# Kernel tuning notes

Measured on AMD Instinct MI355X. Metric: run time of the kernel, lower is better.

Reference implementation:

```python
import jax, jax.numpy as jnp
import numpy as np

DIM = 2048
HEAD = 256
SEQ = 4096

def setup_inputs() -> dict:
    key = jax.random.key(0)
    ks = jax.random.split(key, 7)
    s = 1.0 / np.sqrt(DIM)
    return {
        "marketStateBatch": jax.random.normal(ks[0], (SEQ, DIM), dtype=jnp.float32),
        "Wq": jax.random.uniform(ks[1], (HEAD, DIM), jnp.float32, -s, s),
        "bq": jax.random.uniform(ks[2], (HEAD,), jnp.float32, -s, s),
        "Wk": jax.random.uniform(ks[3], (HEAD, DIM), jnp.float32, -s, s),
        "bk": jax.random.uniform(ks[4], (HEAD,), jnp.float32, -s, s),
        "Wv": jax.random.uniform(ks[5], (HEAD, DIM), jnp.float32, -s, s),
        "bv": jax.random.uniform(ks[6], (HEAD,), jnp.float32, -s, s),
    }

def reference(marketStateBatch, Wq, bq, Wk, bk, Wv, bv):
    x = marketStateBatch  # [S, D]
    q = x @ Wq.T + bq     # [S, H]
    k = x @ Wk.T + bk     # [S, H]
    v = x @ Wv.T + bv     # [S, H]
    # NOTE: original scales by sqrt(dimensionSize), the INPUT dim, not head dim.
    scores = (q @ k.T) * (1.0 / np.sqrt(DIM))  # [S, S]
    S = x.shape[0]
    causal = jnp.tril(jnp.ones((S, S), dtype=bool))
    scores = jnp.where(causal, scores, -jnp.inf)
    attn = jax.nn.softmax(scores, axis=-1)
    # torch.nan_to_num(attn, 0.0): rows are never all -inf here (diag kept),
    # but replicate the op faithfully.
    attn = jnp.nan_to_num(attn, nan=0.0)
    return attn @ v  # [S, H]
```

## Files before the change

kernel.cpp:

```cpp
#include <hip/hip_runtime.h>
#include <stdint.h>

#define SEQ 4096
#define DIMK 2048
#define HD 256

typedef __attribute__((ext_vector_type(8))) short bf16x8;
typedef __attribute__((ext_vector_type(4))) short u16x4;
typedef __attribute__((ext_vector_type(4))) float f32x4;
typedef __attribute__((ext_vector_type(16))) float f32x16;
typedef unsigned short u16;
typedef unsigned int u32;

#define BAR() asm volatile("s_barrier" ::: "memory")
#define VMCNT(n) asm volatile("s_waitcnt vmcnt(" #n ")" ::: "memory")

__device__ __forceinline__ u16 f2bf(float f) {
    u32 u = __float_as_uint(f);
    u += 0x7FFFu + ((u >> 16) & 1u);
    return (u16)(u >> 16);
}

__device__ __forceinline__ float bf2f(u16 h) {
    u32 u = ((u32)h) << 16;
    return __uint_as_float(u);
}

__device__ __forceinline__ bf16x8 pack8(f32x4 a0, f32x4 a1) {
    bf16x8 v8;
    v8[0]=(short)f2bf(a0[0]); v8[1]=(short)f2bf(a0[1]);
    v8[2]=(short)f2bf(a0[2]); v8[3]=(short)f2bf(a0[3]);
    v8[4]=(short)f2bf(a1[0]); v8[5]=(short)f2bf(a1[1]);
    v8[6]=(short)f2bf(a1[2]); v8[7]=(short)f2bf(a1[3]);
    return v8;
}

__device__ __forceinline__ void gl16(const void* g, void* l) {
    __builtin_amdgcn_global_load_lds(
        (const __attribute__((address_space(1))) void*)g,
        (__attribute__((address_space(3))) void*)l, 16, 0, 0);
}

__device__ __forceinline__ u32 cvtpk(float lo, float hi) {
    u32 d;
    asm("v_cvt_pk_bf16_f32 %0, %1, %2" : "=v"(d) : "v"(lo), "v"(hi));
    return d;
}

__device__ __forceinline__ void plswap(u32& x, u32& y) {
#if __has_builtin(__builtin_amdgcn_permlane32_swap)
    typedef int i32x2 __attribute__((ext_vector_type(2)));
    i32x2 r = __builtin_amdgcn_permlane32_swap((int)x, (int)y, false, false);
    x = (u32)r[0]; y = (u32)r[1];
#else
    asm("v_permlane32_swap_b32 %0, %1" : "+v"(x), "+v"(y));
#endif
}

__global__ __launch_bounds__(256) void cvt_all2(
    const float* __restrict__ x, const float* __restrict__ Wq,
    const float* __restrict__ Wk, const float* __restrict__ Wv,
    u16* __restrict__ xb_sw, u16* __restrict__ wb_sw)
{
    const int y = blockIdx.y;
    int i = blockIdx.x * 256 + threadIdx.x;
    int stride = gridDim.x * 256;
    if (y == 0) {
        for (; i < SEQ*DIMK/8; i += stride) {
            int row = i >> 8, c8 = i & 255;
            f32x4 a0 = *(const f32x4*)(x + (size_t)row*DIMK + c8*8);
            f32x4 a1 = *(const f32x4*)(x + (size_t)row*DIMK + c8*8 + 4);
            int mt = row >> 6, rl = row & 63, kt = c8 >> 3, sl = c8 & 7;
            size_t dst = ((size_t)(mt*32 + kt))*4096 + rl*64 + ((sl ^ (rl&7))*8);
            *(bf16x8*)(xb_sw + dst) = pack8(a0, a1);
        }
    } else {
        const float* W = (y==1) ? Wq : (y==2) ? Wk : Wv;
        for (; i < HD*DIMK/8; i += stride) {
            int row = i >> 8, c8 = i & 255;
            f32x4 a0 = *(const f32x4*)(W + (size_t)row*DIMK + c8*8);
            f32x4 a1 = *(const f32x4*)(W + (size_t)row*DIMK + c8*8 + 4);
            int gr = (y-1)*256 + row;
            int nt = gr >> 7, rl = gr & 127, kt = c8 >> 3, sl = c8 & 7;
            size_t dst = ((size_t)(nt*32 + kt))*8192 + rl*64 + ((sl ^ (rl&7))*8);
            *(bf16x8*)(wb_sw + dst) = pack8(a0, a1);
        }
    }
}

__global__ __launch_bounds__(256, 2) void qkv_gemm2b(
    const u16* __restrict__ xb_sw, const u16* __restrict__ wb_sw,
    const float* __restrict__ bq, const float* __restrict__ bk,
    const float* __restrict__ bv,
    u16* __restrict__ qb, u16* __restrict__ kb_t, u16* __restrict__ vt_t)
{
    __shared__ char T[3][24576];

    const int tid = threadIdx.x;
    const int lane = tid & 63;
    const int w = tid >> 6;
    const int r = lane & 15, g = lane >> 4;
    const int wr = w >> 1, wc = w & 1;
    const int mt = blockIdx.x;
    const int y  = blockIdx.y;
    const int z  = y >> 1;
    const float* bias = (z==0) ? bq : (z==1) ? bk : bv;

    const u16* abase = xb_sw + (size_t)mt*32*4096;
    const u16* bbase = wb_sw + (size_t)y*32*8192;

    f32x4 zero = {0.f,0.f,0.f,0.f};
    f32x4 acc[2][4];
    #pragma unroll
    for (int m = 0; m < 2; ++m)
        #pragma unroll
        for (int n = 0; n < 4; ++n) acc[m][n] = zero;

    auto stage = [&](int b, int kt) {
        const u16* ag = abase + (size_t)kt*4096 + w*1024 + lane*8;
        const u16* bg = bbase + (size_t)kt*8192 + w*2048 + lane*8;
        char* al = T[b] + w*2048;
        char* bl = T[b] + 8192 + w*4096;
        gl16(ag,        al);
        gl16(ag + 512,  al + 1024);
        gl16(bg,        bl);
        gl16(bg + 512,  bl + 1024);
        gl16(bg + 1024, bl + 2048);
        gl16(bg + 1536, bl + 3072);
    };

    stage(0, 0);
    stage(1, 1);

    for (int kt = 0; kt < 32; ++kt) {
        if (kt < 31) { VMCNT(6); } else { VMCNT(0); }
        BAR();
        if (kt + 2 < 32) stage((kt + 2) % 3, kt + 2);
        const char* A = T[kt % 3];
        const char* B = T[kt % 3] + 8192;
        __builtin_amdgcn_s_setprio(1);
        #pragma unroll
        for (int kc = 0; kc < 2; ++kc) {
            bf16x8 af[2], bfr[4];
            #pragma unroll
            for (int m = 0; m < 2; ++m) {
                int arow = wr*32 + m*16 + r;
                af[m] = *(const bf16x8*)(A + arow*128 + (((kc*4+g) ^ (arow&7)) << 4));
            }
            #pragma unroll
            for (int n = 0; n < 4; ++n) {
                int brow = wc*64 + n*16 + r;
                bfr[n] = *(const bf16x8*)(B + brow*128 + (((kc*4+g) ^ (brow&7)) << 4));
            }
            #pragma unroll
            for (int m = 0; m < 2; ++m)
                #pragma unroll
                for (int n = 0; n < 4; ++n)
                    acc[m][n] = __builtin_amdgcn_mfma_f32_16x16x32_bf16(
                        af[m], bfr[n], acc[m][n], 0, 0, 0);
        }
        __builtin_amdgcn_s_setprio(0);
    }

    const int m0 = mt*64, n0 = y*128;
    const float qs = 0.03187936f;
    if (z == 0) {
        #pragma unroll
        for (int n = 0; n < 4; ++n) {
            int hc = (n0 + wc*64 + n*16 + r) & 255;
            float bcol = bias[hc];
            #pragma unroll
            for (int m = 0; m < 2; ++m) {
                int row0 = m0 + wr*32 + m*16 + g*4;
                #pragma unroll
                for (int j = 0; j < 4; ++j)
                    qb[(size_t)(row0+j)*HD + hc] = f2bf((acc[m][n][j] + bcol) * qs);
            }
        }
    } else if (z == 1) {
        #pragma unroll
        for (int n = 0; n < 4; ++n) {
            int hc = (n0 + wc*64 + n*16 + r) & 255;
            float bcol = bias[hc];
            #pragma unroll
            for (int m = 0; m < 2; ++m) {
                int row0 = m0 + wr*32 + m*16 + g*4;
                #pragma unroll
                for (int j = 0; j < 4; ++j) {
                    int rowj = row0 + j;
                    int t = rowj >> 5, rl = rowj & 31;
                    kb_t[(size_t)t*8192 + rl*256 + (((hc>>3) ^ (rl&7))*8) + (hc&7)]
                        = f2bf(acc[m][n][j] + bcol);
                }
            }
        }
    } else {
        #pragma unroll
        for (int n = 0; n < 4; ++n) {
            int hc = (n0 + wc*64 + n*16 + r) & 255;
            float bcol = bias[hc];
            #pragma unroll
            for (int m = 0; m < 2; ++m) {
                int kv0 = m0 + wr*32 + m*16 + g*4;
                int t = kv0 >> 5, kl = kv0 & 31;
                u16x4 pk;
                #pragma unroll
                for (int j = 0; j < 4; ++j) pk[j] = (short)f2bf(acc[m][n][j] + bcol);
                *(u16x4*)(vt_t + (size_t)t*8192 + hc*32 +
                          (((kl>>3) ^ (hc&3) ^ ((hc>>2)&3))*8) + (kl&7)) = pk;
            }
        }
    }
}

__global__ __launch_bounds__(256, 2) void attn_part10(
    const u16* __restrict__ qb, const u16* __restrict__ kb_t,
    const u16* __restrict__ vt_t,
    u16* __restrict__ po, float* __restrict__ pm, float* __restrict__ pl,
    int C)
{
    __shared__ char Kb[2][16384];
    __shared__ char Vb[2][16384];

    const int pid = blockIdx.x;
    int Q = 0, a0 = 0;
    for (int k = 0; k < 32; ++k) {
        int nsk = (4*k + 4 + C - 1) / C;
        if (pid < a0 + nsk) { Q = k; break; }
        a0 += nsk;
    }
    const int s  = pid - a0;
    const int nt = 4*Q + 4;
    const int t0 = s*C;
    const int t1 = min(t0 + C, nt);

    const int tid = threadIdx.x;
    const int L = tid & 63;
    const int w = tid >> 6;
    const int l31 = L & 31;
    const int h   = L >> 5;
    const int qg  = Q*128 + w*32 + l31;
    const int vsw = (l31 & 3) ^ ((l31 >> 2) & 3);
    const int kx  = l31 & 7;

    auto stageK = [&](int t, int b) {
        const u16* kg = kb_t + (size_t)t*8192 + w*2048 + L*8;
        char* kl = Kb[b] + w*4096;
        #pragma unroll
        for (int i = 0; i < 4; ++i) gl16(kg + i*512, kl + i*1024);
    };
    auto stageV = [&](int t, int b) {
        const u16* vg = vt_t + (size_t)t*8192 + w*2048 + L*8;
        char* vl = Vb[b] + w*4096;
        #pragma unroll
        for (int i = 0; i < 4; ++i) gl16(vg + i*512, vl + i*1024);
    };

    stageK(t0, t0 & 1);
    stageK(min(t0 + 1, t1 - 1), (t0 + 1) & 1);
    stageV(t0, t0 & 1);

    bf16x8 qf[16];
    {
        const u16* qp = qb + (size_t)qg*HD + h*8;
        #pragma unroll
        for (int c = 0; c < 16; ++c) qf[c] = *(const bf16x8*)(qp + c*16);
    }

    f32x16 o[8];
    #pragma unroll
    for (int ht = 0; ht < 8; ++ht)
        #pragma unroll
        for (int e = 0; e < 16; ++e) o[ht][e] = 0.f;
    float lsum = 0.f;
    bf16x8 pp0, pp1;

    auto finish_tile = [&](f32x16& sv, int t) {
        if (t*32 + 31 > Q*128 + w*32) {
            #pragma unroll
            for (int e = 0; e < 16; ++e) {
                int kvr = (e & 3) + 8*(e >> 2) + 4*h;
                if (t*32 + kvr > qg) sv[e] = -__builtin_inff();
            }
        }
        #pragma unroll
        for (int e = 0; e < 16; ++e) sv[e] = exp2f(sv[e]);
        float r0 = ((sv[0]+sv[1])+(sv[2]+sv[3])) + ((sv[4]+sv[5])+(sv[6]+sv[7]));
        float r1 = ((sv[8]+sv[9])+(sv[10]+sv[11])) + ((sv[12]+sv[13])+(sv[14]+sv[15]));
        lsum += r0 + r1;
        {
            union { u32 wd[4]; bf16x8 v8; } up;
            u32 A = cvtpk(sv[0],  sv[1]),  B = cvtpk(sv[2],  sv[3]);
            u32 Cc= cvtpk(sv[4],  sv[5]),  D = cvtpk(sv[6],  sv[7]);
            plswap(A, Cc); plswap(B, D);
            up.wd[0]=A; up.wd[1]=B; up.wd[2]=Cc; up.wd[3]=D;
            pp0 = up.v8;
        }
        {
            union { u32 wd[4]; bf16x8 v8; } up;
            u32 A1 = cvtpk(sv[8],  sv[9]),  B1 = cvtpk(sv[10], sv[11]);
            u32 C1 = cvtpk(sv[12], sv[13]), D1 = cvtpk(sv[14], sv[15]);
            plswap(A1, C1); plswap(B1, D1);
            up.wd[0]=A1; up.wd[1]=B1; up.wd[2]=C1; up.wd[3]=D1;
            pp1 = up.v8;
        }
    };

    {
        VMCNT(8);
        BAR();
        const char* K = Kb[t0 & 1];
        #define LDK(c) (*(const bf16x8*)(K + l31*512 + (((2*(c) + h) ^ kx) << 4)))
        f32x16 sv;
        #pragma unroll
        for (int e = 0; e < 16; ++e) sv[e] = 0.f;
        __builtin_amdgcn_s_setprio(1);
        {
            bf16x8 kk0 = LDK(0), kk1 = LDK(1);
            #pragma unroll
            for (int c = 0; c < 16; ++c) {
                bf16x8 kc = (c & 1) ? kk1 : kk0;
                sv = __builtin_amdgcn_mfma_f32_32x32x16_bf16(kc, qf[c], sv, 0, 0, 0);
                if (c + 2 < 16) { if (c & 1) kk1 = LDK(c + 2); else kk0 = LDK(c + 2); }
            }
        }
        #undef LDK
        __builtin_amdgcn_s_setprio(0);
        finish_tile(sv, t0);
        BAR();
        stageK(min(t0 + 2, t1 - 1), t0 & 1);
        stageV(min(t0 + 1, t1 - 1), (t0 + 1) & 1);
    }

    for (int t = t0 + 1; t < t1; ++t) {
        VMCNT(8);
        BAR();
        const char* K  = Kb[t & 1];
        const char* Vp = Vb[(t - 1) & 1];

        #define LDK(c) (*(const bf16x8*)(K + l31*512 + (((2*(c) + h) ^ kx) << 4)))
        f32x16 sv;
        #pragma unroll
        for (int e = 0; e < 16; ++e) sv[e] = 0.f;
        __builtin_amdgcn_s_setprio(1);
        {
            bf16x8 kk0 = LDK(0), kk1 = LDK(1);
            #pragma unroll
            for (int c = 0; c < 16; ++c) {
                bf16x8 kc = (c & 1) ? kk1 : kk0;
                sv = __builtin_amdgcn_mfma_f32_32x32x16_bf16(kc, qf[c], sv, 0, 0, 0);
                if (c + 2 < 16) { if (c & 1) kk1 = LDK(c + 2); else kk0 = LDK(c + 2); }
                {
                    const int ht = c & 7;
                    const int sl = ((c < 8) ? h : (2 + h)) ^ vsw;
                    bf16x8 vf = *(const bf16x8*)(Vp + (ht*32 + l31)*64 + (sl << 4));
                    o[ht] = __builtin_amdgcn_mfma_f32_32x32x16_bf16(
                        vf, (c < 8) ? pp0 : pp1, o[ht], 0, 0, 0);
                }
            }
        }
        #undef LDK
        __builtin_amdgcn_s_setprio(0);

        finish_tile(sv, t);

        BAR();
        stageK(min(t + 2, t1 - 1), t & 1);
        stageV(min(t + 1, t1 - 1), (t + 1) & 1);
    }

    VMCNT(0);
    BAR();
    {
        const char* Vp = Vb[(t1 - 1) & 1];
        __builtin_amdgcn_s_setprio(1);
        #pragma unroll
        for (int ht = 0; ht < 8; ++ht) {
            bf16x8 vf0 = *(const bf16x8*)(Vp + (ht*32 + l31)*64 + (((h)     ^ vsw) << 4));
            bf16x8 vf1 = *(const bf16x8*)(Vp + (ht*32 + l31)*64 + (((2 + h) ^ vsw) << 4));
            o[ht] = __builtin_amdgcn_mfma_f32_32x32x16_bf16(vf0, pp0, o[ht], 0, 0, 0);
            o[ht] = __builtin_amdgcn_mfma_f32_32x32x16_bf16(vf1, pp1, o[ht], 0, 0, 0);
        }
        __builtin_amdgcn_s_setprio(0);
    }

    float lrun = lsum + __shfl_xor(lsum, 32);
    if (h == 0) {
        pm[(size_t)pid*128 + w*32 + l31] = 0.f;
        pl[(size_t)pid*128 + w*32 + l31] = lrun;
    }
    u16* op = po + ((size_t)pid*128 + w*32 + l31) * 256;
    #pragma unroll
    for (int ht = 0; ht < 8; ++ht)
        #pragma unroll
        for (int j = 0; j < 8; ++j) {
            u32 pk = (u32)f2bf(o[ht][2*j]) | ((u32)f2bf(o[ht][2*j+1]) << 16);
            int hdb = ht*32 + (j & 1)*2 + (j >> 1)*8 + 4*h;
            *(u32*)(op + hdb) = pk;
        }
}

__global__ __launch_bounds__(256) void attn_combine5(
    const u16* __restrict__ po, const float* __restrict__ pm,
    const float* __restrict__ pl, float* __restrict__ out, int C)
{
    const int tid = threadIdx.x;
    const int row = blockIdx.x * 16 + (tid >> 4);
    const int cg  = tid & 15;
    const int Q   = row >> 7, rr = row & 127;
    const int nt  = 4*Q + 4;
    const int ns  = (nt + C - 1) / C;
    int pid0 = 0;
    for (int k = 0; k < Q; ++k) pid0 += (4*k + 4 + C - 1) / C;

    float M = -1e30f;
    for (int s = 0; s < ns; ++s)
        M = fmaxf(M, pm[(size_t)(pid0+s)*128 + rr]);

    float lt = 0.f;
    f32x4 acc[4];
    f32x4 zero = {0.f,0.f,0.f,0.f};
    #pragma unroll
    for (int v = 0; v < 4; ++v) acc[v] = zero;

    for (int s = 0; s < ns; ++s) {
        float ms  = pm[(size_t)(pid0+s)*128 + rr];
        float wgt = exp2f(ms - M);
        lt += wgt * pl[(size_t)(pid0+s)*128 + rr];
        const u16* p = po + ((size_t)(pid0+s)*128 + rr)*256 + cg*16;
        #pragma unroll
        for (int v = 0; v < 4; ++v) {
            u16x4 pv = *(const u16x4*)(p + v*4);
            #pragma unroll
            for (int e = 0; e < 4; ++e)
                acc[v][e] += wgt * bf2f((u16)pv[e]);
        }
    }
    float inv = 1.f / lt;
    f32x4* op = (f32x4*)(out + (size_t)row*256 + cg*16);
    #pragma unroll
    for (int v = 0; v < 4; ++v) op[v] = acc[v] * inv;
}

extern "C" void kernel_launch(void* const* d_in, const int* in_sizes, int n_in,
                              void* d_out, int out_size, void* d_ws, size_t ws_size,
                              hipStream_t stream) {
    const float* x  = (const float*)d_in[0];
    const float* Wq = (const float*)d_in[1];
    const float* bq = (const float*)d_in[2];
    const float* Wk = (const float*)d_in[3];
    const float* bk = (const float*)d_in[4];
    const float* Wv = (const float*)d_in[5];
    const float* bv = (const float*)d_in[6];
    float* out = (float*)d_out;

    const size_t xb_bytes  = (size_t)SEQ * DIMK * 2;
    const size_t wb_bytes  = (size_t)768 * DIMK * 2;
    const size_t qkv_bytes = (size_t)SEQ * HD * 2;
    const size_t base = xb_bytes + wb_bytes + 3*qkv_bytes;

    int C = 64;
    size_t npid = 0;
    const int cand[4] = {5, 8, 16, 64};
    for (int ci = 0; ci < 4; ++ci) {
        int c = cand[ci];
        size_t np = 0;
        for (int k = 0; k < 32; ++k) np += (size_t)(4*k + 4 + c - 1) / c;
        size_t need = base + np * ((size_t)128*256*2 + 2*128*4);
        if (need <= ws_size) { C = c; npid = np; break; }
        if (ci == 3) { C = c; npid = np; }
    }

    char* p = (char*)d_ws;
    u16* xb_sw = (u16*)p; p += xb_bytes;
    u16* wb_sw = (u16*)p; p += wb_bytes;
    u16* qbuf  = (u16*)p; p += qkv_bytes;
    u16* kb_t  = (u16*)p; p += qkv_bytes;
    u16* vt_t  = (u16*)p; p += qkv_bytes;
    u16* po    = (u16*)p; p += npid * 128 * 256 * 2;
    float* pm  = (float*)p; p += npid * 128 * 4;
    float* pl  = (float*)p; p += npid * 128 * 4;

    cvt_all2<<<dim3(512, 4), 256, 0, stream>>>(x, Wq, Wk, Wv, xb_sw, wb_sw);

    qkv_gemm2b<<<dim3(SEQ/64, 6), 256, 0, stream>>>(
        xb_sw, wb_sw, bq, bk, bv, qbuf, kb_t, vt_t);

    attn_part10<<<(int)npid, 256, 0, stream>>>(
        qbuf, kb_t, vt_t, po, pm, pl, C);

    attn_combine5<<<SEQ/16, 256, 0, stream>>>(po, pm, pl, out, C);
}
```

Measured before the change: 75.94 us.

## Replace split-KV partial writes and combine with float atomics into transposed accumulator

Each split-KV partition now atomically adds its unnormalized output and row sum straight into a transposed fp32 accumulator, instead of writing bf16 partials plus max and sum for a separate combine pass. A zeroing kernel and a small normalize/transpose kernel replace the combine kernel, and C is fixed to 5. The aim is to cut partial-buffer traffic and the combine work. The cost is many float atomics per element plus an extra zeroing launch. The atomics also make the result order-nondeterministic, though that is safe here only because the fixed max of zero makes the partials directly summable.

Result: slower. 119.5 us (+57.3%).

```diff
diff --git a/kernel.cpp b/kernel.cpp
--- a/kernel.cpp
+++ b/kernel.cpp
@@ -19,11 +19,6 @@
     u32 u = __float_as_uint(f);
     u += 0x7FFFu + ((u >> 16) & 1u);
     return (u16)(u >> 16);
-}
-
-__device__ __forceinline__ float bf2f(u16 h) {
-    u32 u = ((u32)h) << 16;
-    return __uint_as_float(u);
 }
 
 __device__ __forceinline__ bf16x8 pack8(f32x4 a0, f32x4 a1) {
@@ -55,6 +50,22 @@
 #else
     asm("v_permlane32_swap_b32 %0, %1" : "+v"(x), "+v"(y));
 #endif
+}
+
+__device__ __forceinline__ void atomadd(float* p, float v) {
+    unsafeAtomicAdd(p, v);
+}
+
+__global__ __launch_bounds__(256) void zero_buf(float* __restrict__ ot,
+                                                float* __restrict__ pl)
+{
+    const int n4 = (HD*SEQ)/4;
+    f32x4 z = {0.f,0.f,0.f,0.f};
+    int i = blockIdx.x * 256 + threadIdx.x;
+    int stride = gridDim.x * 256;
+    for (; i < n4; i += stride) *(f32x4*)(ot + (size_t)i*4) = z;
+    for (i = blockIdx.x * 256 + threadIdx.x; i < SEQ/4; i += stride)
+        *(f32x4*)(pl + (size_t)i*4) = z;
 }
 
 __global__ __launch_bounds__(256) void cvt_all2(
@@ -213,10 +224,10 @@
     }
 }
 
-__global__ __launch_bounds__(256, 2) void attn_part10(
+__global__ __launch_bounds__(256, 2) void attn_part12(
     const u16* __restrict__ qb, const u16* __restrict__ kb_t,
     const u16* __restrict__ vt_t,
-    u16* __restrict__ po, float* __restrict__ pm, float* __restrict__ pl,
+    float* __restrict__ ot, float* __restrict__ pl,
     int C)
 {
     __shared__ char Kb[2][16384];
@@ -384,62 +395,47 @@
         __builtin_amdgcn_s_setprio(0);
     }
 
-    float lrun = lsum + __shfl_xor(lsum, 32);
-    if (h == 0) {
-        pm[(size_t)pid*128 + w*32 + l31] = 0.f;
-        pl[(size_t)pid*128 + w*32 + l31] = lrun;
-    }
-    u16* op = po + ((size_t)pid*128 + w*32 + l31) * 256;
+    atomadd(&pl[qg], lsum);
     #pragma unroll
     for (int ht = 0; ht < 8; ++ht)
         #pragma unroll
-        for (int j = 0; j < 8; ++j) {
-            u32 pk = (u32)f2bf(o[ht][2*j]) | ((u32)f2bf(o[ht][2*j+1]) << 16);
-            int hdb = ht*32 + (j & 1)*2 + (j >> 1)*8 + 4*h;
-            *(u32*)(op + hdb) = pk;
-        }
-}
-
-__global__ __launch_bounds__(256) void attn_combine5(
-    const u16* __restrict__ po, const float* __restrict__ pm,
-    const float* __restrict__ pl, float* __restrict__ out, int C)
+        for (int e = 0; e < 16; ++e) {
+            int hd = ht*32 + (e & 3) + 8*(e >> 2) + 4*h;
+            atomadd(ot + (size_t)hd*SEQ + qg, o[ht][e]);
+        }
+}
+
+__global__ __launch_bounds__(256) void attn_norm(
+    const float* __restrict__ ot, const float* __restrict__ pl,
+    float* __restrict__ out)
 {
-    const int tid = threadIdx.x;
-    const int row = blockIdx.x * 16 + (tid >> 4);
-    const int cg  = tid & 15;
-    const int Q   = row >> 7, rr = row & 127;
-    const int nt  = 4*Q + 4;
-    const int ns  = (nt + C - 1) / C;
-    int pid0 = 0;
-    for (int k = 0; k < Q; ++k) pid0 += (4*k + 4 + C - 1) / C;
-
-    float M = -1e30f;
-    for (int s = 0; s < ns; ++s)
-        M = fmaxf(M, pm[(size_t)(pid0+s)*128 + rr]);
-
-    float lt = 0.f;
-    f32x4 acc[4];
-    f32x4 zero = {0.f,0.f,0.f,0.f};
+    __shared__ float tr[64][257];
+    const int tid  = threadIdx.x;
+    const int row0 = blockIdx.x * 64;
+    const int rl = tid & 63;
+    const int hq = tid >> 6;
+
+    #pragma unroll 4
+    for (int h2 = 0; h2 < 64; ++h2) {
+        int hd = hq*64 + h2;
+        tr[rl][hd] = ot[(size_t)hd*SEQ + row0 + rl];
+    }
+    __syncthreads();
+
+    const int orow = tid >> 2;
+    const int c0   = (tid & 3) * 64;
+    float inv = 1.f / pl[row0 + orow];
+    float* op = out + (size_t)(row0 + orow)*HD + c0;
     #pragma unroll
-    for (int v = 0; v < 4; ++v) acc[v] = zero;
-
-    for (int s = 0; s < ns; ++s) {
-        float ms  = pm[(size_t)(pid0+s)*128 + rr];
-        float wgt = exp2f(ms - M);
-        lt += wgt * pl[(size_t)(pid0+s)*128 + rr];
-        const u16* p = po + ((size_t)(pid0+s)*128 + rr)*256 + cg*16;
-        #pragma unroll
-        for (int v = 0; v < 4; ++v) {
-            u16x4 pv = *(const u16x4*)(p + v*4);
-            #pragma unroll
-            for (int e = 0; e < 4; ++e)
-                acc[v][e] += wgt * bf2f((u16)pv[e]);
-        }
-    }
-    float inv = 1.f / lt;
-    f32x4* op = (f32x4*)(out + (size_t)row*256 + cg*16);
-    #pragma unroll
-    for (int v = 0; v < 4; ++v) op[v] = acc[v] * inv;
+    for (int c = 0; c < 64; c += 4) {
+        f32x4 v;
+        v[0] = tr[orow][c0 + c];
+        v[1] = tr[orow][c0 + c + 1];
+        v[2] = tr[orow][c0 + c + 2];
+        v[3] = tr[orow][c0 + c + 3];
+        v[0] *= inv; v[1] *= inv; v[2] *= inv; v[3] *= inv;
+        *(f32x4*)(op + c) = v;
+    }
 }
 
 extern "C" void kernel_launch(void* const* d_in, const int* in_sizes, int n_in,
@@ -457,19 +453,12 @@
     const size_t xb_bytes  = (size_t)SEQ * DIMK * 2;
     const size_t wb_bytes  = (size_t)768 * DIMK * 2;
     const size_t qkv_bytes = (size_t)SEQ * HD * 2;
-    const size_t base = xb_bytes + wb_bytes + 3*qkv_bytes;
-
-    int C = 64;
+    const size_t ot_bytes  = (size_t)HD * SEQ * 4;
+    const size_t pl_bytes  = (size_t)SEQ * 4;
+
+    const int C = 5;
     size_t npid = 0;
-    const int cand[4] = {5, 8, 16, 64};
-    for (int ci = 0; ci < 4; ++ci) {
-        int c = cand[ci];
-        size_t np = 0;
-        for (int k = 0; k < 32; ++k) np += (size_t)(4*k + 4 + c - 1) / c;
-        size_t need = base + np * ((size_t)128*256*2 + 2*128*4);
-        if (need <= ws_size) { C = c; npid = np; break; }
-        if (ci == 3) { C = c; npid = np; }
-    }
+    for (int k = 0; k < 32; ++k) npid += (size_t)(4*k + 4 + C - 1) / C;
 
     char* p = (char*)d_ws;
     u16* xb_sw = (u16*)p; p += xb_bytes;
@@ -477,17 +466,18 @@
     u16* qbuf  = (u16*)p; p += qkv_bytes;
     u16* kb_t  = (u16*)p; p += qkv_bytes;
     u16* vt_t  = (u16*)p; p += qkv_bytes;
-    u16* po    = (u16*)p; p += npid * 128 * 256 * 2;
-    float* pm  = (float*)p; p += npid * 128 * 4;
-    float* pl  = (float*)p; p += npid * 128 * 4;
+    float* ot  = (float*)p; p += ot_bytes;
+    float* pl  = (float*)p; p += pl_bytes;
+
+    zero_buf<<<512, 256, 0, stream>>>(ot, pl);
 
     cvt_all2<<<dim3(512, 4), 256, 0, stream>>>(x, Wq, Wk, Wv, xb_sw, wb_sw);
 
     qkv_gemm2b<<<dim3(SEQ/64, 6), 256, 0, stream>>>(
         xb_sw, wb_sw, bq, bk, bv, qbuf, kb_t, vt_t);
 
-    attn_part10<<<(int)npid, 256, 0, stream>>>(
-        qbuf, kb_t, vt_t, po, pm, pl, C);
-
-    attn_combine5<<<SEQ/16, 256, 0, stream>>>(po, pm, pl, out, C);
-}
+    attn_part12<<<(int)npid, 256, 0, stream>>>(
+        qbuf, kb_t, vt_t, ot, pl, C);
+
+    attn_norm<<<SEQ/64, 256, 0, stream>>>(ot, pl, out);
+}
```
